# Performance work log

Measured on AMD Instinct MI355X. Metric: run time of the kernel, lower is better.

The kernel has to match this reference:

```python
import jax, jax.numpy as jnp
import numpy as np

IN_CH = 1280
NUM_HEADS = 8
DIM_DOWN = 5
CUT_RATE = 4
SCALE = (IN_CH // NUM_HEADS) ** -0.5  # faithful to original: uses in_ch//num_heads


def setup_inputs() -> dict:
    key = jax.random.key(0)
    ks = jax.random.split(key, 5)
    B, N = 4, 4096
    C = IN_CH // DIM_DOWN  # 256
    x = jax.random.normal(ks[0], (B, N, IN_CH), dtype=jnp.float32)
    Wd = jax.random.normal(ks[1], (IN_CH, C), dtype=jnp.float32) * (IN_CH ** -0.5)
    Wqkv = jax.random.normal(ks[2], (C, 3 * C), dtype=jnp.float32) * (C ** -0.5)
    Wup = jax.random.normal(ks[3], (C, IN_CH), dtype=jnp.float32) * (C ** -0.5)
    bup = jnp.zeros((IN_CH,), dtype=jnp.float32)
    return {"x": x, "Wd": Wd, "Wqkv": Wqkv, "Wup": Wup, "bup": bup}


def reference(x, Wd, Wqkv, Wup, bup):
    # dim-down projection (dropout is identity at rate 0 / eval)
    h = x @ Wd                                  # [B, N, C]
    B, N, C = h.shape
    H = NUM_HEADS
    hd = C // H
    blk = N // CUT_RATE
    qkv = (h @ Wqkv).reshape(B, N, 3, H, hd)
    qkv = jnp.transpose(qkv, (2, 0, 3, 1, 4))   # [3, B, H, N, hd]
    q, k, v = qkv[0], qkv[1], qkv[2]
    # block-diagonal local attention: split N into CUT_RATE independent chunks
    q = q.reshape(B, H, CUT_RATE, blk, hd)
    k = k.reshape(B, H, CUT_RATE, blk, hd)
    v = v.reshape(B, H, CUT_RATE, blk, hd)
    attn = jnp.einsum('bhcqd,bhckd->bhcqk', q, k) * SCALE
    attn = jax.nn.softmax(attn, axis=-1)
    o = jnp.einsum('bhcqk,bhckd->bhcqd', attn, v)
    # torch cat over chunks along token dim, then merge heads: [B, N, C]
    o = jnp.transpose(o, (0, 2, 3, 1, 4)).reshape(B, N, C)
    return o @ Wup + bup
```

## Files before the change

kernel.cpp:

```cpp
#include <hip/hip_runtime.h>

typedef unsigned short u16;
typedef unsigned int u32;
typedef u16 u16x4 __attribute__((ext_vector_type(4)));
typedef u16 u16x8 __attribute__((ext_vector_type(8)));
typedef __bf16 bf16x8 __attribute__((ext_vector_type(8)));
typedef float f32x4 __attribute__((ext_vector_type(4)));

__device__ __forceinline__ u16 f2bf(float f) {
  union { float f; unsigned u; } c; c.f = f;
  unsigned u = c.u;
  return (u16)((u + 0x7fff + ((u >> 16) & 1)) >> 16);
}

__device__ __forceinline__ float fexp2(float x) {
  float r; asm("v_exp_f32 %0, %1" : "=v"(r) : "v"(x)); return r;
}

__device__ __forceinline__ u32 cvtpk(float lo, float hi) {
  u32 r;
  asm("v_cvt_pk_bf16_f32 %0, %1, %2" : "=v"(r) : "v"(lo), "v"(hi));
  return r;
}

__device__ __forceinline__ void lds16(const u16* g, u16* l) {
  __builtin_amdgcn_global_load_lds(
      (const __attribute__((address_space(1))) unsigned int*)g,
      (__attribute__((address_space(3))) unsigned int*)l, 16, 0, 0);
}

#define CEXP (0.07905694150420949f * 1.4426950408889634f)

#define BAR()  do { asm volatile("" ::: "memory"); \
                    __builtin_amdgcn_s_barrier(); \
                    asm volatile("" ::: "memory"); } while (0)
#define VMC(n) asm volatile("s_waitcnt vmcnt(" #n ")" ::: "memory")

#define PREP_W (1280 * 256 + 768 * 256 + 1280 * 256)

__global__ __launch_bounds__(256)
void prep_w(const float* __restrict__ Wd, const float* __restrict__ Wqkv,
            const float* __restrict__ Wup,
            u16* __restrict__ WdC, u16* __restrict__ WqkvT,
            u16* __restrict__ WupT) {
  int id = blockIdx.x * 256 + threadIdx.x;
  if (id < 1280 * 256) {
    WdC[id] = f2bf(Wd[id]);
    return;
  }
  id -= 1280 * 256;
  if (id < 768 * 256) {
    int n = id >> 8, c = id & 255;
    float v = Wqkv[(size_t)c * 768 + n];
    if (n < 256) v *= CEXP;
    WqkvT[id] = f2bf(v);
    return;
  }
  id -= 768 * 256;
  if (id < 1280 * 256) {
    int n = id >> 8, c = id & 255;
    WupT[id] = f2bf(Wup[(size_t)c * 1280 + n]);
  }
}

__global__ __launch_bounds__(256)
void wpt_xcast(const u16* __restrict__ WqkvT, const u16* __restrict__ WdC,
               u16* __restrict__ WpT,
               const float* __restrict__ X, u16* __restrict__ Xb, int n8)
{
  __shared__ u16 As[128][64];
  __shared__ u16 Bs[128][64];

  if (blockIdx.x >= 60) {
    int id = (blockIdx.x - 60) * 256 + threadIdx.x;
    if (id < n8) {
      const float4* src = (const float4*)(X + (size_t)id * 8);
      float4 lo = src[0], hi = src[1];
      u16x8 v;
      v[0]=f2bf(lo.x); v[1]=f2bf(lo.y); v[2]=f2bf(lo.z); v[3]=f2bf(lo.w);
      v[4]=f2bf(hi.x); v[5]=f2bf(hi.y); v[6]=f2bf(hi.z); v[7]=f2bf(hi.w);
      *(u16x8*)(Xb + (size_t)id * 8) = v;
    }
    return;
  }

  const int tid  = threadIdx.x;
  const int wave = tid >> 6, lane = tid & 63;
  const int quad = lane >> 4, l16 = lane & 15;
  const int rsw  = l16 & 7;
  const int ssw  = ((lane & 7) ^ (lane >> 3)) << 3;
  const int band = blockIdx.x / 10, nblk = blockIdx.x % 10;
  const int m0 = band * 128, n0 = nblk * 128;
  const int wr = (wave >> 1) * 64, wc = (wave & 1) * 64;
  const int K = 256, N = 1280;

  f32x4 acc[4][4];
#pragma unroll
  for (int i = 0; i < 4; i++)
#pragma unroll
    for (int j = 0; j < 4; j++) acc[i][j] = f32x4{0.f, 0.f, 0.f, 0.f};

  for (int k0 = 0; k0 < K; k0 += 64) {
#pragma unroll
    for (int it = 0; it < 4; it++) {
      int r0 = wave * 32 + it * 8;
      lds16(&WqkvT[(size_t)(m0 + r0 + (lane >> 3)) * K + k0 + ssw],
            &As[r0][0] + lane * 8);
      lds16(&WdC[(size_t)(n0 + r0 + (lane >> 3)) * K + k0 + ssw],
            &Bs[r0][0] + lane * 8);
    }
    __syncthreads();
#pragma unroll
    for (int ks = 0; ks < 64; ks += 32) {
      bf16x8 af[4], bfr[4];
#pragma unroll
      for (int i = 0; i < 4; i++)
        af[i] = *(const bf16x8*)&As[wr + i * 16 + l16][(((ks >> 3) + quad) ^ rsw) << 3];
#pragma unroll
      for (int j = 0; j < 4; j++)
        bfr[j] = *(const bf16x8*)&Bs[wc + j * 16 + l16][(((ks >> 3) + quad) ^ rsw) << 3];
#pragma unroll
      for (int i = 0; i < 4; i++)
#pragma unroll
        for (int j = 0; j < 4; j++)
          acc[i][j] = __builtin_amdgcn_mfma_f32_16x16x32_bf16(af[i], bfr[j], acc[i][j], 0, 0, 0);
    }
    __syncthreads();
  }

#pragma unroll
  for (int i = 0; i < 4; i++)
#pragma unroll
    for (int j = 0; j < 4; j++) {
      int col = n0 + wc + j * 16 + l16;
#pragma unroll
      for (int r = 0; r < 4; r++) {
        int row = m0 + wr + i * 16 + quad * 4 + r;
        WpT[(size_t)row * N + col] = f2bf(acc[i][j][r]);
      }
    }
}

template <int AF32>
__global__ __launch_bounds__(256)
void gemm_bt(const void* __restrict__ Av,
             const u16* __restrict__ BT,
             u16* __restrict__ Cb, float* __restrict__ Cf,
             const float* __restrict__ bias,
             int M, int N, int K)
{
  __shared__ u16 As[128][64];
  __shared__ u16 Bs[128][64];
  const int tid  = threadIdx.x;
  const int wave = tid >> 6, lane = tid & 63;
  const int quad = lane >> 4, l16 = lane & 15;
  const int rsw  = l16 & 7;
  const int ssw  = ((lane & 7) ^ (lane >> 3)) << 3;

  const int nb = N >> 7, mb = M >> 7;
  int band, nblk;
  if ((mb & 7) == 0) {
    int xcd = blockIdx.x & 7, slot = blockIdx.x >> 3;
    band = xcd + 8 * (slot / nb);
    nblk = slot % nb;
  } else {
    band = blockIdx.x / nb;
    nblk = blockIdx.x % nb;
  }
  const int m0 = band * 128, n0 = nblk * 128;
  const int wr = (wave >> 1) * 64, wc = (wave & 1) * 64;
  const u16*   A16 = (const u16*)Av;
  const float* A32 = (const float*)Av;

  f32x4 acc[4][4];
#pragma unroll
  for (int i = 0; i < 4; i++)
#pragma unroll
    for (int j = 0; j < 4; j++) acc[i][j] = f32x4{0.f, 0.f, 0.f, 0.f};

  for (int k0 = 0; k0 < K; k0 += 64) {
    if constexpr (AF32) {
#pragma unroll
      for (int it = 0; it < 4; it++) {
        int idx = tid + it * 256;
        int r = idx >> 3;
        const float* src = &A32[(size_t)(m0 + r) * K + k0 + ((idx & 7) << 3)];
        float4 lo = *(const float4*)src;
        float4 hi = *(const float4*)(src + 4);
        u16x8 v;
        v[0]=f2bf(lo.x); v[1]=f2bf(lo.y); v[2]=f2bf(lo.z); v[3]=f2bf(lo.w);
        v[4]=f2bf(hi.x); v[5]=f2bf(hi.y); v[6]=f2bf(hi.z); v[7]=f2bf(hi.w);
        *(u16x8*)&As[r][((idx & 7) ^ (r & 7)) << 3] = v;
      }
#pragma unroll
      for (int it = 0; it < 4; it++) {
        int r0 = wave * 32 + it * 8;
        lds16(&BT[(size_t)(n0 + r0 + (lane >> 3)) * K + k0 + ssw],
              &Bs[r0][0] + lane * 8);
      }
    } else {
#pragma unroll
      for (int it = 0; it < 4; it++) {
        int r0 = wave * 32 + it * 8;
        lds16(&A16[(size_t)(m0 + r0 + (lane >> 3)) * K + k0 + ssw],
              &As[r0][0] + lane * 8);
        lds16(&BT[(size_t)(n0 + r0 + (lane >> 3)) * K + k0 + ssw],
              &Bs[r0][0] + lane * 8);
      }
    }
    __syncthreads();
#pragma unroll
    for (int ks = 0; ks < 64; ks += 32) {
      bf16x8 af[4], bfr[4];
#pragma unroll
      for (int i = 0; i < 4; i++)
        af[i] = *(const bf16x8*)&As[wr + i * 16 + l16][(((ks >> 3) + quad) ^ rsw) << 3];
#pragma unroll
      for (int j = 0; j < 4; j++)
        bfr[j] = *(const bf16x8*)&Bs[wc + j * 16 + l16][(((ks >> 3) + quad) ^ rsw) << 3];
#pragma unroll
      for (int i = 0; i < 4; i++)
#pragma unroll
        for (int j = 0; j < 4; j++)
          acc[i][j] = __builtin_amdgcn_mfma_f32_16x16x32_bf16(af[i], bfr[j], acc[i][j], 0, 0, 0);
    }
    __syncthreads();
  }

#pragma unroll
  for (int i = 0; i < 4; i++) {
#pragma unroll
    for (int j = 0; j < 4; j++) {
      int col = n0 + wc + j * 16 + l16;
      float bv = bias ? bias[col] : 0.0f;
#pragma unroll
      for (int r = 0; r < 4; r++) {
        int row = m0 + wr + i * 16 + quad * 4 + r;
        float v = acc[i][j][r] + bv;
        if (Cf) Cf[(size_t)row * N + col] = v;
        else    Cb[(size_t)row * N + col] = f2bf(v);
      }
    }
  }
}

#define LDA_(d, ib) { _Pragma("unroll") for (int i = 0; i < 4; i++) \
  _Pragma("unroll") for (int ks = 0; ks < 2; ks++) \
    af[i*2+ks] = *(const bf16x8*)&As[d][wm][(ib+i)*16 + l16][((ks*4+quad) ^ rsw) << 3]; }

#define LDB_(d, dst, jp) { _Pragma("unroll") for (int j = 0; j < 2; j++) \
  _Pragma("unroll") for (int ks = 0; ks < 2; ks++) \
    dst[j*2+ks] = *(const bf16x8*)&Bs[d][bh][br + (jp*2+j)*16 + l16][((ks*4+quad) ^ rsw) << 3]; }

#define MM_(ib, jp, breg) { __builtin_amdgcn_s_setprio(1); \
  _Pragma("unroll") for (int i = 0; i < 4; i++) \
  _Pragma("unroll") for (int j = 0; j < 2; j++) \
  _Pragma("unroll") for (int ks = 0; ks < 2; ks++) \
    acc[ib+i][jp*2+j] = __builtin_amdgcn_mfma_f32_16x16x32_bf16( \
        af[i*2+ks], breg[j*2+ks], acc[ib+i][jp*2+j], 0, 0, 0); \
  __builtin_amdgcn_s_setprio(0); }

__global__ __launch_bounds__(512, 2)
void gemm_bt256(const u16* __restrict__ A16, const u16* __restrict__ BT,
                u16* __restrict__ Cb, int M, int N, int K)
{
  __shared__ __align__(16) u16 As[2][2][128][64];
  __shared__ __align__(16) u16 Bs[2][2][128][64];
  const int tid  = threadIdx.x;
  const int wave = tid >> 6, lane = tid & 63;
  const int quad = lane >> 4, l16 = lane & 15;
  const int wm = wave >> 2, wn = wave & 3;
  const int bh = wn >> 1, br = (wn & 1) * 64;
  const int rsw = l16 & 7;

  const int nb = N >> 8, mb = M >> 8;
  int band, nblk;
  if ((mb & 7) == 0) {
    int xcd = blockIdx.x & 7, slot = blockIdx.x >> 3;
    band = xcd + 8 * (slot / nb);
    nblk = slot % nb;
  } else {
    band = blockIdx.x / nb;
    nblk = blockIdx.x % nb;
  }
  const int m0 = band * 256, n0 = nblk * 256;
  const int NT = K >> 6;

  const int srow = tid >> 3;
  const int scol = ((tid & 7) ^ (srow & 7)) << 3;

  auto stageA = [&](int t, int h) {
    const int d = t & 1;
    const size_t g = (size_t)(m0 + h * 128 + srow) * K + (t << 6) + scol;
    lds16(&A16[g], &As[d][h][0][0] + tid * 8);
    lds16(&A16[g + (size_t)64 * K], &As[d][h][64][0] + tid * 8);
  };
  auto stageB = [&](int t, int h) {
    const int d = t & 1;
    const size_t g = (size_t)(n0 + h * 128 + srow) * K + (t << 6) + scol;
    lds16(&BT[g], &Bs[d][h][0][0] + tid * 8);
    lds16(&BT[g + (size_t)64 * K], &Bs[d][h][64][0] + tid * 8);
  };

  bf16x8 af[8], b0[4], b1[4];
  f32x4 acc[8][4];
#pragma unroll
  for (int i = 0; i < 8; i++)
#pragma unroll
    for (int j = 0; j < 4; j++) acc[i][j] = f32x4{0.f, 0.f, 0.f, 0.f};

  stageA(0, 0); stageA(0, 1); stageB(0, 0); stageB(0, 1); stageA(1, 0);
  VMC(2);
  BAR();

  const int nIter = NT >> 1;
  for (int it = 0; it < nIter; ++it) {
    const int t0 = it * 2, t1 = t0 + 1;
    const bool more  = (t0 + 2 < NT);
    const bool more1 = (t1 + 2 < NT);

    LDA_(0, 0); LDB_(0, b0, 0);
    stageA(t1, 1);
    BAR(); MM_(0, 0, b0); BAR();
    LDB_(0, b1, 1);
    stageB(t1, 0);
    BAR(); MM_(0, 1, b1); BAR();
    LDA_(0, 4);
    stageB(t1, 1);
    BAR(); MM_(4, 1, b1); BAR();
    if (more) stageA(t0 + 2, 0);
    BAR(); MM_(4, 0, b0);
    if (more) { VMC(2); } else { VMC(0); }
    BAR();

    LDA_(1, 0); LDB_(1, b0, 0);
    if (more) stageA(t0 + 2, 1);
    BAR(); MM_(0, 0, b0); BAR();
    LDB_(1, b1, 1);
    if (more) stageB(t0 + 2, 0);
    BAR(); MM_(0, 1, b1); BAR();
    LDA_(1, 4);
    if (more) stageB(t0 + 2, 1);
    BAR(); MM_(4, 1, b1); BAR();
    if (more1) stageA(t1 + 2, 0);
    BAR(); MM_(4, 0, b0);
    if (it + 1 < nIter) {
      if (more1) { VMC(2); } else { VMC(0); }
      BAR();
    }
  }

#pragma unroll
  for (int i = 0; i < 8; i++) {
#pragma unroll
    for (int j = 0; j < 4; j++) {
      const int col = n0 + wn * 64 + j * 16 + l16;
#pragma unroll
      for (int r = 0; r < 4; r++) {
        const int row = m0 + wm * 128 + i * 16 + quad * 4 + r;
        Cb[(size_t)row * N + col] = f2bf(acc[i][j][r]);
      }
    }
  }
}

__global__ __launch_bounds__(256)
void vtrans(const u16* __restrict__ qkv, u16* __restrict__ vT)
{
  __shared__ u16 T[32][72];
  const int tid   = threadIdx.x;
  const int kt    = blockIdx.x;
  const int head  = blockIdx.y >> 2;
  const int chunk = blockIdx.y & 3;
  const int b     = blockIdx.z;
  const size_t rowbase = (size_t)b * 4096 + chunk * 1024 + kt * 64;

  const int tok = tid >> 2;
  const int d8  = (tid & 3) << 3;
  u16x8 vv = *(const u16x8*)&qkv[(rowbase + tok) * 768 + 512 + head * 32 + d8];
  const int rot = (tok + (d8 >> 3)) & 7;
#pragma unroll
  for (int jj = 0; jj < 8; jj++) {
    int j = (jj + rot) & 7;
    T[d8 + j][tok] = vv[j];
  }
  __syncthreads();
  const int d = tid >> 3;
  const int s = tid & 7;
  const int base = ((s >> 2) << 5) + ((s & 3) << 2);
  u16x4 lo = *(const u16x4*)&T[d][base];
  u16x4 hi = *(const u16x4*)&T[d][base + 16];
  u16x8 o8;
  o8[0]=lo[0]; o8[1]=lo[1]; o8[2]=lo[2]; o8[3]=lo[3];
  o8[4]=hi[0]; o8[5]=hi[1]; o8[6]=hi[2]; o8[7]=hi[3];
  size_t obase = ((size_t)((b * 4 + chunk) * 8 + head)) * 32768
               + (size_t)d * 1024 + kt * 64 + s * 8;
  *(u16x8*)&vT[obase] = o8;
}

__global__ __launch_bounds__(256)
void attn_kernel(const u16* __restrict__ qkv, const u16* __restrict__ vT,
                 u16* __restrict__ o)
{
  __shared__ __align__(16) u16 Ks[4][64][32];
  __shared__ __align__(16) u16 VTs[4][32][64];

  const int tid  = threadIdx.x;
  const int wave = tid >> 6, lane = tid & 63;
  const int quad = lane >> 4, l16 = lane & 15;
  const int gid   = blockIdx.x;
  const int qb    = gid >> 7;
  const int g     = gid & 127;
  const int head  = g >> 4;
  const int chunk = (g >> 2) & 3;
  const int b     = g & 3;
  const size_t rowbase = (size_t)b * 4096 + chunk * 1024;
  const int tok0 = qb * 128 + wave * 32;

  const int kkey = tid >> 2;
  const int kd8  = (tid & 3) << 3;
  const int vr   = tid >> 3;
  const int vs   = tid & 7;
  const int vsl  = (vs ^ (vr & 7)) << 3;
  const size_t vbase = ((size_t)((b * 4 + chunk) * 8 + head)) * 32768
                     + (size_t)vr * 1024 + vsl;

  auto stageKV = [&](int kb, int buf) {
    lds16(&qkv[(rowbase + kb * 64 + kkey) * 768 + 256 + head * 32 + kd8],
          &Ks[buf][0][0] + tid * 8);
    lds16(&vT[vbase + (size_t)kb * 64], &VTs[buf][0][0] + tid * 8);
  };

  stageKV(0, 0);

  bf16x8 qf[2];
#pragma unroll
  for (int qt = 0; qt < 2; qt++)
    qf[qt] = *(const bf16x8*)&qkv[(rowbase + tok0 + qt * 16 + l16) * 768 + head * 32 + quad * 8];

  stageKV(1, 1);

  bf16x8 onesb;
  {
    union { u16x8 u; bf16x8 v; } c;
#pragma unroll
    for (int i = 0; i < 8; i++) c.u[i] = 0x3F80;
    onesb = c.v;
  }

  f32x4 Oacc[2][2], Osum[2];
#pragma unroll
  for (int qt = 0; qt < 2; qt++) {
    Osum[qt] = f32x4{0.f, 0.f, 0.f, 0.f};
#pragma unroll
    for (int nd = 0; nd < 2; nd++) Oacc[qt][nd] = f32x4{0.f, 0.f, 0.f, 0.f};
  }

  VMC(2);
  BAR();

  for (int kb = 0; kb < 16; kb++) {
    const int cur = kb & 3;
    if (kb + 2 < 16) stageKV(kb + 2, (kb + 2) & 3);

    bf16x8 kf[4];
#pragma unroll
    for (int kt = 0; kt < 4; kt++)
      kf[kt] = *(const bf16x8*)&Ks[cur][kt * 16 + l16][quad * 8];

    f32x4 ST[4][2];
    __builtin_amdgcn_s_setprio(1);
#pragma unroll
    for (int kt = 0; kt < 4; kt++)
#pragma unroll
      for (int qt = 0; qt < 2; qt++)
        ST[kt][qt] = __builtin_amdgcn_mfma_f32_16x16x32_bf16(kf[kt], qf[qt], f32x4{0.f,0.f,0.f,0.f}, 0, 0, 0);
    __builtin_amdgcn_s_setprio(0);

    u32 pw[2][4][2];
#pragma unroll
    for (int qt = 0; qt < 2; qt++)
#pragma unroll
      for (int kt = 0; kt < 4; kt++) {
        float p0 = fexp2(ST[kt][qt][0]);
        float p1 = fexp2(ST[kt][qt][1]);
        float p2 = fexp2(ST[kt][qt][2]);
        float p3 = fexp2(ST[kt][qt][3]);
        pw[qt][kt][0] = cvtpk(p0, p1);
        pw[qt][kt][1] = cvtpk(p2, p3);
      }

#pragma unroll
    for (int ks = 0; ks < 2; ks++) {
      bf16x8 vf[2];
#pragma unroll
      for (int nd = 0; nd < 2; nd++)
        vf[nd] = *(const bf16x8*)&VTs[cur][nd * 16 + l16][((ks * 4 + quad) ^ (l16 & 7)) << 3];
      __builtin_amdgcn_s_setprio(1);
#pragma unroll
      for (int qt = 0; qt < 2; qt++) {
        union { u32 w[4]; bf16x8 v; } pu;
        pu.w[0] = pw[qt][2 * ks][0];
        pu.w[1] = pw[qt][2 * ks][1];
        pu.w[2] = pw[qt][2 * ks + 1][0];
        pu.w[3] = pw[qt][2 * ks + 1][1];
#pragma unroll
        for (int nd = 0; nd < 2; nd++)
          Oacc[qt][nd] = __builtin_amdgcn_mfma_f32_16x16x32_bf16(pu.v, vf[nd], Oacc[qt][nd], 0, 0, 0);
        Osum[qt] = __builtin_amdgcn_mfma_f32_16x16x32_bf16(pu.v, onesb, Osum[qt], 0, 0, 0);
      }
      __builtin_amdgcn_s_setprio(0);
    }

    if (kb < 15) {
      if (kb + 2 < 16) { VMC(2); } else { VMC(0); }
      BAR();
    }
  }

#pragma unroll
  for (int qt = 0; qt < 2; qt++)
#pragma unroll
    for (int r = 0; r < 4; r++) {
      float inv = 1.0f / Osum[qt][r];
      size_t row = rowbase + tok0 + qt * 16 + quad * 4 + r;
#pragma unroll
      for (int nd = 0; nd < 2; nd++) {
        int col = head * 32 + nd * 16 + l16;
        o[row * 256 + col] = f2bf(Oacc[qt][nd][r] * inv);
      }
    }
}

extern "C" void kernel_launch(void* const* d_in, const int* in_sizes, int n_in,
                              void* d_out, int out_size, void* d_ws, size_t ws_size,
                              hipStream_t stream)
{
  const float* x    = (const float*)d_in[0];
  const float* Wd   = (const float*)d_in[1];
  const float* Wqkv = (const float*)d_in[2];
  const float* Wup  = (const float*)d_in[3];
  const float* bup  = (const float*)d_in[4];
  float* out = (float*)d_out;

  const int M = 4 * 4096;

  u16* WdC   = (u16*)d_ws;
  u16* WqkvT = WdC   + 1280 * 256;
  u16* WupT  = WqkvT + 768 * 256;
  u16* WpT   = WupT  + 1280 * 256;
  u16* qkv   = WpT   + 768 * 1280;
  u16* ob    = qkv   + (size_t)M * 768;
  u16* xb    = ob    + (size_t)M * 256;
  u16* vT    = xb;

  const size_t need = ((size_t)(1280*256 + 768*256 + 1280*256 + 768*1280)
                       + (size_t)M * (768 + 256 + 1280)) * sizeof(u16);
  const bool use_xb = ws_size >= need;

  prep_w<<<(PREP_W + 255) / 256, 256, 0, stream>>>(
      Wd, Wqkv, Wup, WdC, WqkvT, WupT);

  const int n8 = use_xb ? (M * 1280 / 8) : 0;
  wpt_xcast<<<60 + (n8 + 255) / 256, 256, 0, stream>>>(
      WqkvT, WdC, WpT, x, xb, n8);

  if (use_xb) {
    gemm_bt256<<<dim3((768 / 256) * (M / 256)), 512, 0, stream>>>(
        xb, WpT, qkv, M, 768, 1280);
  } else {
    gemm_bt<1><<<dim3((768 / 128) * (M / 128)), 256, 0, stream>>>(
        (const void*)x, WpT, qkv, nullptr, nullptr, M, 768, 1280);
  }

  vtrans<<<dim3(16, 32, 4), 256, 0, stream>>>(qkv, vT);

  attn_kernel<<<dim3(1024), 256, 0, stream>>>(qkv, vT, ob);

  gemm_bt<0><<<dim3((1280 / 128) * (M / 128)), 256, 0, stream>>>(
      (const void*)ob, WupT, nullptr, out, bup, M, 1280, 256);
}
```

Measured before the change: 259.8 us.

## Fuse V transpose into QKV GEMM epilogue and write head-major Q/K/V panels

The QKV GEMM epilogue now writes Q and K straight into per-(batch,chunk,head) contiguous panels and transposes V through shared memory into the vT layout. This removes the separate vtrans launch and its extra round trip through global memory. Attention loads K and Q from contiguous panels instead of strided rows of the 768-wide qkv buffer. In exchange, Q/K stores in the epilogue are scalar 2-byte strided writes. The fallback path gains a slow scalar repack kernel that uses the output buffer as scratch.

```diff
diff --git a/kernel.cpp b/kernel.cpp
--- a/kernel.cpp
+++ b/kernel.cpp
@@ -261,11 +261,13 @@
   __builtin_amdgcn_s_setprio(0); }
 
 __global__ __launch_bounds__(512, 2)
-void gemm_bt256(const u16* __restrict__ A16, const u16* __restrict__ BT,
-                u16* __restrict__ Cb, int M, int N, int K)
+void gemm_qkv(const u16* __restrict__ A16, const u16* __restrict__ BT,
+              u16* __restrict__ qT, u16* __restrict__ kT,
+              u16* __restrict__ vT, int M, int N, int K)
 {
-  __shared__ __align__(16) u16 As[2][2][128][64];
-  __shared__ __align__(16) u16 Bs[2][2][128][64];
+  __shared__ __align__(16) u16 SH[2][2][2][128][64];
+  auto& As = SH[0];
+  auto& Bs = SH[1];
   const int tid  = threadIdx.x;
   const int wave = tid >> 6, lane = tid & 63;
   const int quad = lane >> 4, l16 = lane & 15;
@@ -273,16 +275,10 @@
   const int bh = wn >> 1, br = (wn & 1) * 64;
   const int rsw = l16 & 7;
 
-  const int nb = N >> 8, mb = M >> 8;
-  int band, nblk;
-  if ((mb & 7) == 0) {
-    int xcd = blockIdx.x & 7, slot = blockIdx.x >> 3;
-    band = xcd + 8 * (slot / nb);
-    nblk = slot % nb;
-  } else {
-    band = blockIdx.x / nb;
-    nblk = blockIdx.x % nb;
-  }
+  const int nb = N >> 8;
+  const int xcd = blockIdx.x & 7, slot = blockIdx.x >> 3;
+  const int band = xcd + 8 * (slot / nb);
+  const int nblk = slot % nb;
   const int m0 = band * 256, n0 = nblk * 256;
   const int NT = K >> 6;
 
@@ -350,57 +346,85 @@
     }
   }
 
-#pragma unroll
-  for (int i = 0; i < 8; i++) {
-#pragma unroll
-    for (int j = 0; j < 4; j++) {
-      const int col = n0 + wn * 64 + j * 16 + l16;
-#pragma unroll
-      for (int r = 0; r < 4; r++) {
-        const int row = m0 + wm * 128 + i * 16 + quad * 4 + r;
-        Cb[(size_t)row * N + col] = f2bf(acc[i][j][r]);
-      }
-    }
+  const int b_ = m0 >> 12, chunk_ = (m0 >> 10) & 3;
+  const int ghb = (b_ * 4 + chunk_) * 8;
+
+  if (n0 == 512) {
+    u16* T = &SH[0][0][0][0][0];
+    BAR();
+#pragma unroll
+    for (int i = 0; i < 8; i++)
+#pragma unroll
+      for (int j = 0; j < 4; j++) {
+        const int vcol = wn * 64 + j * 16 + l16;
+        const int tok4 = (wm * 128 + i * 16 + quad * 4) ^ ((vcol & 7) << 2);
+        uint2 w;
+        w.x = cvtpk(acc[i][j][0], acc[i][j][1]);
+        w.y = cvtpk(acc[i][j][2], acc[i][j][3]);
+        *(uint2*)&T[vcol * 256 + tok4] = w;
+      }
+    __syncthreads();
+    const int ktb = (m0 & 1023) >> 6;
+    const int s   = tid & 7;
+    const int hd0 = tid >> 3;
+#pragma unroll
+    for (int u = 0; u < 4; u++) {
+      const int hd = u * 64 + hd0;
+      const int head = hd >> 5, d = hd & 31;
+      const int x = (hd & 7) << 2;
+      const size_t gb = (size_t)(ghb + head) * 32768 + (size_t)d * 1024 + s * 8;
+#pragma unroll
+      for (int kt4 = 0; kt4 < 4; kt4++) {
+        const int base = kt4 * 64 + ((s >> 2) << 5) + ((s & 3) << 2);
+        u16x4 lo = *(const u16x4*)&T[hd * 256 + (base ^ x)];
+        u16x4 hi = *(const u16x4*)&T[hd * 256 + ((base + 16) ^ x)];
+        u16x8 o8;
+        o8[0]=lo[0]; o8[1]=lo[1]; o8[2]=lo[2]; o8[3]=lo[3];
+        o8[4]=hi[0]; o8[5]=hi[1]; o8[6]=hi[2]; o8[7]=hi[3];
+        *(u16x8*)&vT[gb + (size_t)(ktb + kt4) * 64] = o8;
+      }
+    }
+  } else {
+    u16* P = (n0 == 0) ? qT : kT;
+    const int tic0 = (m0 & 1023) + wm * 128 + quad * 4;
+#pragma unroll
+    for (int i = 0; i < 8; i++)
+#pragma unroll
+      for (int j = 0; j < 4; j++) {
+        const int c255 = wn * 64 + j * 16 + l16;
+        const int head = c255 >> 5, d = c255 & 31;
+        u16* Pg = P + (size_t)(ghb + head) * 32768 + d;
+#pragma unroll
+        for (int r = 0; r < 4; r++) {
+          const int tic = tic0 + i * 16 + r;
+          Pg[(size_t)tic * 32] = f2bf(acc[i][j][r]);
+        }
+      }
   }
 }
 
 __global__ __launch_bounds__(256)
-void vtrans(const u16* __restrict__ qkv, u16* __restrict__ vT)
+void repack_fb(const u16* __restrict__ qkv, u16* __restrict__ qT,
+               u16* __restrict__ kT, u16* __restrict__ vT)
 {
-  __shared__ u16 T[32][72];
-  const int tid   = threadIdx.x;
-  const int kt    = blockIdx.x;
-  const int head  = blockIdx.y >> 2;
-  const int chunk = blockIdx.y & 3;
-  const int b     = blockIdx.z;
-  const size_t rowbase = (size_t)b * 4096 + chunk * 1024 + kt * 64;
-
-  const int tok = tid >> 2;
-  const int d8  = (tid & 3) << 3;
-  u16x8 vv = *(const u16x8*)&qkv[(rowbase + tok) * 768 + 512 + head * 32 + d8];
-  const int rot = (tok + (d8 >> 3)) & 7;
-#pragma unroll
-  for (int jj = 0; jj < 8; jj++) {
-    int j = (jj + rot) & 7;
-    T[d8 + j][tok] = vv[j];
-  }
-  __syncthreads();
-  const int d = tid >> 3;
-  const int s = tid & 7;
-  const int base = ((s >> 2) << 5) + ((s & 3) << 2);
-  u16x4 lo = *(const u16x4*)&T[d][base];
-  u16x4 hi = *(const u16x4*)&T[d][base + 16];
-  u16x8 o8;
-  o8[0]=lo[0]; o8[1]=lo[1]; o8[2]=lo[2]; o8[3]=lo[3];
-  o8[4]=hi[0]; o8[5]=hi[1]; o8[6]=hi[2]; o8[7]=hi[3];
-  size_t obase = ((size_t)((b * 4 + chunk) * 8 + head)) * 32768
-               + (size_t)d * 1024 + kt * 64 + s * 8;
-  *(u16x8*)&vT[obase] = o8;
+  int id = blockIdx.x * 256 + threadIdx.x;
+  int tok = id >> 3, head = id & 7;
+  int b = tok >> 12, chunk = (tok >> 10) & 3, tic = tok & 1023;
+  int gh = (b * 4 + chunk) * 8 + head;
+  int kt = tic >> 6, k64 = tic & 63, b32 = k64 >> 5, k32 = k64 & 31;
+  int s = b32 * 4 + ((k32 >> 2) & 3);
+  int j = (k32 & 3) | ((k32 >> 4) << 2);
+  size_t src = (size_t)tok * 768 + head * 32;
+  for (int d = 0; d < 32; d++) {
+    qT[(size_t)gh * 32768 + (size_t)tic * 32 + d] = qkv[src + d];
+    kT[(size_t)gh * 32768 + (size_t)tic * 32 + d] = qkv[src + 256 + d];
+    vT[(size_t)gh * 32768 + (size_t)d * 1024 + kt * 64 + s * 8 + j] = qkv[src + 512 + d];
+  }
 }
 
 __global__ __launch_bounds__(256)
-void attn_kernel(const u16* __restrict__ qkv, const u16* __restrict__ vT,
-                 u16* __restrict__ o)
+void attn_kernel(const u16* __restrict__ qT, const u16* __restrict__ kT,
+                 const u16* __restrict__ vT, u16* __restrict__ o)
 {
   __shared__ __align__(16) u16 Ks[4][64][32];
   __shared__ __align__(16) u16 VTs[4][32][64];
@@ -414,20 +438,18 @@
   const int head  = g >> 4;
   const int chunk = (g >> 2) & 3;
   const int b     = g & 3;
+  const int gh    = (b * 4 + chunk) * 8 + head;
   const size_t rowbase = (size_t)b * 4096 + chunk * 1024;
   const int tok0 = qb * 128 + wave * 32;
 
-  const int kkey = tid >> 2;
-  const int kd8  = (tid & 3) << 3;
   const int vr   = tid >> 3;
   const int vs   = tid & 7;
   const int vsl  = (vs ^ (vr & 7)) << 3;
-  const size_t vbase = ((size_t)((b * 4 + chunk) * 8 + head)) * 32768
-                     + (size_t)vr * 1024 + vsl;
+  const size_t vbase = (size_t)gh * 32768 + (size_t)vr * 1024 + vsl;
+  const size_t kbase = (size_t)gh * 32768;
 
   auto stageKV = [&](int kb, int buf) {
-    lds16(&qkv[(rowbase + kb * 64 + kkey) * 768 + 256 + head * 32 + kd8],
-          &Ks[buf][0][0] + tid * 8);
+    lds16(&kT[kbase + kb * 2048 + tid * 8], &Ks[buf][0][0] + tid * 8);
     lds16(&vT[vbase + (size_t)kb * 64], &VTs[buf][0][0] + tid * 8);
   };
 
@@ -436,7 +458,7 @@
   bf16x8 qf[2];
 #pragma unroll
   for (int qt = 0; qt < 2; qt++)
-    qf[qt] = *(const bf16x8*)&qkv[(rowbase + tok0 + qt * 16 + l16) * 768 + head * 32 + quad * 8];
+    qf[qt] = *(const bf16x8*)&qT[kbase + (size_t)(tok0 + qt * 16 + l16) * 32 + quad * 8];
 
   stageKV(1, 1);
 
@@ -544,15 +566,17 @@
   float* out = (float*)d_out;
 
   const int M = 4 * 4096;
+  const size_t PANEL = (size_t)128 * 32768;
 
   u16* WdC   = (u16*)d_ws;
   u16* WqkvT = WdC   + 1280 * 256;
   u16* WupT  = WqkvT + 768 * 256;
   u16* WpT   = WupT  + 1280 * 256;
-  u16* qkv   = WpT   + 768 * 1280;
-  u16* ob    = qkv   + (size_t)M * 768;
+  u16* qT    = WpT   + 768 * 1280;
+  u16* kT    = qT    + PANEL;
+  u16* vT    = kT    + PANEL;
+  u16* ob    = vT    + PANEL;
   u16* xb    = ob    + (size_t)M * 256;
-  u16* vT    = xb;
 
   const size_t need = ((size_t)(1280*256 + 768*256 + 1280*256 + 768*1280)
                        + (size_t)M * (768 + 256 + 1280)) * sizeof(u16);
@@ -565,17 +589,21 @@
   wpt_xcast<<<60 + (n8 + 255) / 256, 256, 0, stream>>>(
       WqkvT, WdC, WpT, x, xb, n8);
 
+  const u16 *aq, *ak, *av;
   if (use_xb) {
-    gemm_bt256<<<dim3((768 / 256) * (M / 256)), 512, 0, stream>>>(
-        xb, WpT, qkv, M, 768, 1280);
+    gemm_qkv<<<dim3((768 / 256) * (M / 256)), 512, 0, stream>>>(
+        xb, WpT, qT, kT, vT, M, 768, 1280);
+    aq = qT; ak = kT; av = vT;
   } else {
+    u16* qkv = qT;
     gemm_bt<1><<<dim3((768 / 128) * (M / 128)), 256, 0, stream>>>(
         (const void*)x, WpT, qkv, nullptr, nullptr, M, 768, 1280);
-  }
-
-  vtrans<<<dim3(16, 32, 4), 256, 0, stream>>>(qkv, vT);
-
-  attn_kernel<<<dim3(1024), 256, 0, stream>>>(qkv, vT, ob);
+    u16* s0 = (u16*)d_out;
+    repack_fb<<<(M * 8) / 256, 256, 0, stream>>>(qkv, s0, s0 + PANEL, s0 + 2 * PANEL);
+    aq = s0; ak = s0 + PANEL; av = s0 + 2 * PANEL;
+  }
+
+  attn_kernel<<<dim3(1024), 256, 0, stream>>>(aq, ak, av, ob);
 
   gemm_bt<0><<<dim3((1280 / 128) * (M / 128)), 256, 0, stream>>>(
       (const void*)ob, WupT, nullptr, out, bup, M, 1280, 256);
```

Result: faster. 250.2 us, median of 2 (-3.7%).
